# Kernel optimization log

Hardware: AMD Instinct MI355X
Metric: run time of the kernel (lower is better)

## Reference

```python
import jax, jax.numpy as jnp
import numpy as np

N, E, D, H, ED = 50000, 800000, 128, 4, 64
C = D // H  # per-head channels
EPS = 1e-5


def setup_inputs() -> dict:
    key = jax.random.key(0)
    ks = jax.random.split(key, 16)
    s = 0.05
    return {
        "x": jax.random.normal(ks[0], (N, D), jnp.float32),
        "edge_index": jax.random.randint(ks[1], (2, E), 0, N, jnp.int64 if jax.config.jax_enable_x64 else jnp.int32),
        "edge_attr": jax.random.normal(ks[2], (E, ED), jnp.float32),
        "Wq": jax.random.normal(ks[3], (D, H * C), jnp.float32) * s,
        "bq": jnp.zeros((H * C,), jnp.float32),
        "Wk": jax.random.normal(ks[4], (D, H * C), jnp.float32) * s,
        "bk": jnp.zeros((H * C,), jnp.float32),
        "Wv": jax.random.normal(ks[5], (D, H * C), jnp.float32) * s,
        "bv": jnp.zeros((H * C,), jnp.float32),
        "We": jax.random.normal(ks[6], (ED, H * C), jnp.float32) * s,  # lin_edge, bias=False
        "Wskip": jax.random.normal(ks[7], (D, H * C), jnp.float32) * s,
        "bskip": jnp.zeros((H * C,), jnp.float32),
        "Wbeta": jax.random.normal(ks[8], (3 * H * C, 1), jnp.float32) * s,  # lin_beta, bias=False
        "gamma": jnp.ones((D,), jnp.float32),
        "beta_ln": jnp.zeros((D,), jnp.float32),
    }


def _transformer_conv(x, src, dst, edge_attr, Wq, bq, Wk, bk, Wv, bv, We, Wskip, bskip, Wbeta):
    q = (x @ Wq + bq).reshape(N, H, C)
    k = (x @ Wk + bk).reshape(N, H, C)
    v = (x @ Wv + bv).reshape(N, H, C)
    e = (edge_attr @ We).reshape(E, H, C)
    k_j = k[src] + e                     # [E,H,C]
    v_j = v[src] + e                     # [E,H,C]
    alpha = jnp.einsum("ehc,ehc->eh", q[dst], k_j) / jnp.sqrt(jnp.float32(C))
    # per-destination softmax over incoming edges
    m = jax.ops.segment_max(alpha, dst, num_segments=N)          # [N,H]
    m = jnp.where(jnp.isfinite(m), m, 0.0)
    a = jnp.exp(alpha - m[dst])
    denom = jax.ops.segment_sum(a, dst, num_segments=N)          # [N,H]
    alpha = a / jnp.where(denom > 0, denom, 1.0)[dst]
    out = jax.ops.segment_sum(alpha[:, :, None] * v_j, dst, num_segments=N)  # [N,H,C]
    out = out.reshape(N, H * C)
    # beta-gated skip (beta=True, root_weight)
    x_r = x @ Wskip + bskip
    b = jax.nn.sigmoid(jnp.concatenate([out, x_r, out - x_r], axis=-1) @ Wbeta)  # [N,1]
    return b * x_r + (1.0 - b) * out


def reference(x, edge_index, edge_attr, Wq, bq, Wk, bk, Wv, bv, We, Wskip, bskip, Wbeta, gamma, beta_ln):
    src, dst = edge_index[0], edge_index[1]
    res = _transformer_conv(x, src, dst, edge_attr, Wq, bq, Wk, bk, Wv, bv, We, Wskip, bskip, Wbeta)
    out = jax.nn.gelu(res, approximate=False) + x
    mu = jnp.mean(out, axis=-1, keepdims=True)
    var = jnp.var(out, axis=-1, keepdims=True)
    return (out - mu) * jax.lax.rsqrt(var + EPS) * gamma + beta_ln
```

## Files before the change

kernel.cpp:

```cpp
#include <hip/hip_runtime.h>
#include <math.h>

#define NN 50000
#define EE 800000

typedef __bf16 bf16x8 __attribute__((ext_vector_type(8)));
typedef float f32x4 __attribute__((ext_vector_type(4)));
typedef float f32x2 __attribute__((ext_vector_type(2)));
typedef unsigned short ushort_t;
typedef unsigned int uint_t;

__device__ inline ushort_t f2bf(float f) {
  uint_t u = __float_as_uint(f);
  uint_t r = (u + 0x7fffu + ((u >> 16) & 1u)) >> 16;
  return (ushort_t)r;
}
__device__ inline float bflo(uint_t u) { return __uint_as_float(u << 16); }
__device__ inline float bfhi(uint_t u) { return __uint_as_float(u & 0xffff0000u); }

__device__ inline uint_t pk4_fp8(float a0, float a1, float a2, float a3) {
  a0 = fminf(fmaxf(a0, -448.f), 448.f);
  a1 = fminf(fmaxf(a1, -448.f), 448.f);
  a2 = fminf(fmaxf(a2, -448.f), 448.f);
  a3 = fminf(fmaxf(a3, -448.f), 448.f);
  uint_t lo = (uint_t)__builtin_amdgcn_cvt_pk_fp8_f32(a0, a1, 0, false) & 0xFFFFu;
  uint_t hi = (uint_t)__builtin_amdgcn_cvt_pk_fp8_f32(a2, a3, 0, false) & 0xFFFFu;
  return lo | (hi << 16);
}

__device__ inline void wave_sync() {
  asm volatile("s_waitcnt lgkmcnt(0)" ::: "memory");
  __builtin_amdgcn_wave_barrier();
}

__global__ __launch_bounds__(256) void k_prepA(const float* __restrict__ Wbeta,
                                               float* __restrict__ wcomb,
                                               int* __restrict__ counts) {
  int b = blockIdx.x;
  int o = threadIdx.x;
  if (b == 0) {
    if (o < 128) {
      wcomb[o]       = Wbeta[o]       + Wbeta[256 + o];
      wcomb[128 + o] = Wbeta[128 + o] - Wbeta[256 + o];
    }
  } else {
    int i = (b - 1) * 256 + o;
    if (i < NN) counts[i] = 0;
  }
}

__global__ __launch_bounds__(256) void k_prepB(
    const float* __restrict__ Wq, const float* __restrict__ Wk,
    const float* __restrict__ Wv, const float* __restrict__ Ws,
    const float* __restrict__ bq, const float* __restrict__ bk,
    const float* __restrict__ bv, const float* __restrict__ bs,
    ushort_t* __restrict__ Wbt, float* __restrict__ bcat,
    const float* __restrict__ We, ushort_t* __restrict__ WebT,
    const int* __restrict__ ei, int* __restrict__ counts,
    int* __restrict__ rank) {
  int b = blockIdx.x;
  if (b >= 288) {
    int i = (b - 288) * 256 + threadIdx.x;
    if (i < EE) rank[i] = atomicAdd(&counts[ei[EE + i]], 1);
    return;
  }
  if (b >= 256) {
    int i = (b - 256) * 256 + threadIdx.x;
    int c = i >> 6, k = i & 63;
    WebT[c * 64 + k] = f2bf(We[k * 128 + c]);
    return;
  }
  int i = b * 256 + threadIdx.x;
  int c = i >> 7, k = i & 127;
  float w;
  if (c < 128)      w = Wq[k * 128 + c];
  else if (c < 256) w = Wk[k * 128 + (c - 128)];
  else if (c < 384) w = Wv[k * 128 + (c - 256)];
  else              w = Ws[k * 128 + (c - 384)];
  Wbt[(size_t)c * 128 + k] = f2bf(w);
  if (i < 512) {
    float bb;
    if (i < 128)      bb = bq[i];
    else if (i < 256) bb = bk[i - 128];
    else if (i < 384) bb = bv[i - 256];
    else              bb = bs[i - 384];
    bcat[i] = bb;
  }
}

__global__ __launch_bounds__(256) void k_mmscan(const float* __restrict__ x,
                                                const ushort_t* __restrict__ Wbt,
                                                const float* __restrict__ bcat,
                                                ushort_t* __restrict__ qb,
                                                ushort_t* __restrict__ kb,
                                                ushort_t* __restrict__ vb,
                                                ushort_t* __restrict__ xrb,
                                                int* __restrict__ counts,
                                                int* __restrict__ offsets) {
  __shared__ ushort_t As[128 * 128];
  __shared__ ushort_t Bs[128 * 128];
  int t = threadIdx.x;

  if (blockIdx.x == 391) {
    if (blockIdx.y != 0) return;
    __shared__ int wsum[4];
    __shared__ int s_carry;
    int4* counts4 = (int4*)counts;
    int4* offsets4 = (int4*)offsets;
    int lane = t & 63, w = t >> 6;
    if (t == 0) s_carry = 0;
    __syncthreads();
    for (int base = 0; base < 12500; base += 256) {
      int idx = base + t;
      int4 v = (idx < 12500) ? counts4[idx] : make_int4(0, 0, 0, 0);
      int e1 = v.x, e2 = e1 + v.y, e3 = e2 + v.z, tot = e3 + v.w;
      int s = tot;
#pragma unroll
      for (int off = 1; off < 64; off <<= 1) {
        int u = __shfl_up(s, off);
        if (lane >= off) s += u;
      }
      if (lane == 63) wsum[w] = s;
      __syncthreads();
      if (t == 0) {
        int ex = s_carry;
#pragma unroll
        for (int i = 0; i < 4; ++i) { int tv = wsum[i]; wsum[i] = ex; ex += tv; }
        s_carry = ex;
      }
      __syncthreads();
      int be = wsum[w] + s - tot;
      if (idx < 12500) offsets4[idx] = make_int4(be, be + e1, be + e2, be + e3);
      __syncthreads();
    }
    if (t == 0) offsets[NN] = s_carry;
    return;
  }

  int rb = blockIdx.x * 128;
  int cb = blockIdx.y * 128;

  for (int q = t; q < 2048; q += 256) {
    int r = q >> 4, j = q & 15;
    int row = rb + r;
    float4 f0 = make_float4(0.f, 0.f, 0.f, 0.f), f1 = f0;
    if (row < NN) {
      const float4* xp = (const float4*)&x[(size_t)row * 128 + j * 8];
      f0 = xp[0]; f1 = xp[1];
    }
    uint_t u0 = (uint_t)f2bf(f0.x) | ((uint_t)f2bf(f0.y) << 16);
    uint_t u1 = (uint_t)f2bf(f0.z) | ((uint_t)f2bf(f0.w) << 16);
    uint_t u2 = (uint_t)f2bf(f1.x) | ((uint_t)f2bf(f1.y) << 16);
    uint_t u3 = (uint_t)f2bf(f1.z) | ((uint_t)f2bf(f1.w) << 16);
    int e = r * 128 + ((j * 8) ^ ((r & 7) << 3));
    *(uint4*)&As[e] = make_uint4(u0, u1, u2, u3);
  }
  for (int q = t; q < 2048; q += 256) {
    int c = q >> 4, j = q & 15;
    uint4 w = *(const uint4*)&Wbt[(size_t)(cb + c) * 128 + j * 8];
    int e = c * 128 + ((j * 8) ^ ((c & 7) << 3));
    *(uint4*)&Bs[e] = w;
  }
  __syncthreads();

  int lane = t & 63;
  int wv = t >> 6;
  int wr = wv >> 1, wc = wv & 1;
  int l15 = lane & 15, l4 = lane >> 4;

  f32x4 acc[4][4];
#pragma unroll
  for (int i = 0; i < 4; ++i)
#pragma unroll
    for (int j = 0; j < 4; ++j) acc[i][j] = (f32x4){0.f, 0.f, 0.f, 0.f};

#pragma unroll
  for (int ks = 0; ks < 4; ++ks) {
    int kbv = ks * 32 + l4 * 8;
    bf16x8 af[4], bfr[4];
#pragma unroll
    for (int i = 0; i < 4; ++i) {
      int r = wr * 64 + i * 16 + l15;
      af[i] = *(const bf16x8*)&As[r * 128 + (kbv ^ ((r & 7) << 3))];
    }
#pragma unroll
    for (int j = 0; j < 4; ++j) {
      int c = wc * 64 + j * 16 + l15;
      bfr[j] = *(const bf16x8*)&Bs[c * 128 + (kbv ^ ((c & 7) << 3))];
    }
#pragma unroll
    for (int i = 0; i < 4; ++i)
#pragma unroll
      for (int j = 0; j < 4; ++j)
        acc[i][j] = __builtin_amdgcn_mfma_f32_16x16x32_bf16(af[i], bfr[j], acc[i][j], 0, 0, 0);
  }

  ushort_t* outp = (cb == 0) ? qb : (cb == 128) ? kb : (cb == 256) ? vb : xrb;
#pragma unroll
  for (int j = 0; j < 4; ++j) {
    int colg = wc * 64 + j * 16 + l15;
    float bv = bcat[cb + colg];
#pragma unroll
    for (int i = 0; i < 4; ++i) {
#pragma unroll
      for (int reg = 0; reg < 4; ++reg) {
        int grow = rb + wr * 64 + i * 16 + l4 * 4 + reg;
        if (grow < NN)
          outp[(size_t)grow * 128 + colg] = f2bf(acc[i][j][reg] + bv);
      }
    }
  }
}

__global__ __launch_bounds__(256) void k_fillw(const int* __restrict__ ei,
                                               const int* __restrict__ offsets,
                                               const int* __restrict__ rank,
                                               const float* __restrict__ ea,
                                               const ushort_t* __restrict__ WebT,
                                               int* __restrict__ srcs,
                                               unsigned char* __restrict__ eaWperm) {
  __shared__ ushort_t Bs[128 * 64];
  __shared__ uint_t sOut[64 * 32];
  __shared__ int sP[128];
  int t = threadIdx.x, lane = t & 63, wv = t >> 6;
  int l15 = lane & 15, l4 = lane >> 4;
  int eb = blockIdx.x * 128;

  float4 ld[2][2][2];
#pragma unroll
  for (int T = 0; T < 2; ++T)
#pragma unroll
    for (int ks = 0; ks < 2; ++ks) {
      const float4* p4 = (const float4*)(ea + (size_t)(eb + T * 64 + wv * 16 + l15) * 64
                                         + ks * 32 + l4 * 8);
      ld[T][ks][0] = p4[0];
      ld[T][ks][1] = p4[1];
    }

  if (t < 128) {
    int e = eb + t;
    int d = ei[EE + e];
    int p = offsets[d] + rank[e];
    sP[t] = p;
    srcs[p] = ei[e];
  }
  for (int q = t; q < 1024; q += 256) {
    int c = q >> 3, j = q & 7;
    uint4 w = *(const uint4*)&WebT[(size_t)c * 64 + j * 8];
    *(uint4*)&Bs[c * 64 + ((j * 8) ^ ((c & 7) << 3))] = w;
  }
  __syncthreads();

#pragma unroll
  for (int T = 0; T < 2; ++T) {
    bf16x8 bfr[2];
#pragma unroll
    for (int ks = 0; ks < 2; ++ks) {
      float4 f0 = ld[T][ks][0], f1 = ld[T][ks][1];
      union { uint4 u; bf16x8 v; } ub;
      ub.u.x = (uint_t)f2bf(f0.x) | ((uint_t)f2bf(f0.y) << 16);
      ub.u.y = (uint_t)f2bf(f0.z) | ((uint_t)f2bf(f0.w) << 16);
      ub.u.z = (uint_t)f2bf(f1.x) | ((uint_t)f2bf(f1.y) << 16);
      ub.u.w = (uint_t)f2bf(f1.z) | ((uint_t)f2bf(f1.w) << 16);
      bfr[ks] = ub.v;
    }

    f32x4 acc[8];
#pragma unroll
    for (int i = 0; i < 8; ++i) acc[i] = (f32x4){0.f, 0.f, 0.f, 0.f};
#pragma unroll
    for (int ks = 0; ks < 2; ++ks) {
      int kbv = ks * 32 + l4 * 8;
#pragma unroll
      for (int i = 0; i < 8; ++i) {
        int c = i * 16 + l15;
        bf16x8 af = *(const bf16x8*)&Bs[c * 64 + (kbv ^ ((c & 7) << 3))];
        acc[i] = __builtin_amdgcn_mfma_f32_16x16x32_bf16(af, bfr[ks], acc[i], 0, 0, 0);
      }
    }

    wave_sync();
    uint_t* dst32 = &sOut[wv * 512];
#pragma unroll
    for (int i = 0; i < 8; ++i)
      dst32[l15 * 32 + ((i * 4 + l4) ^ ((l15 & 7) << 2))] =
          pk4_fp8(acc[i][0], acc[i][1], acc[i][2], acc[i][3]);
    wave_sync();

    int elr = lane >> 2, seg = lane & 3;
    int sw = (elr & 7) << 2;
    const uint_t* src32 = &sOut[wv * 512 + elr * 32];
    int w0 = (seg * 8) ^ sw;
    int w1 = (seg * 8 + 4) ^ sw;
    uint4 lo = *(const uint4*)&src32[w0];
    uint4 hi = *(const uint4*)&src32[w1];
    int p = sP[T * 64 + wv * 16 + elr];
    unsigned char* dst = eaWperm + (size_t)p * 128 + seg * 32;
    *(uint4*)dst = lo;
    *(uint4*)(dst + 16) = hi;
  }
}

__global__ __launch_bounds__(256) void k_attn(
    const ushort_t* __restrict__ qb, const ushort_t* __restrict__ xrb,
    const ushort_t* __restrict__ kb, const ushort_t* __restrict__ vb,
    const unsigned char* __restrict__ eaWperm,
    const int* __restrict__ offsets, const int* __restrict__ srcs,
    const float* __restrict__ x, const float* __restrict__ wcomb,
    const float* __restrict__ gamma, const float* __restrict__ beta_ln,
    float* __restrict__ out) {
  __shared__ float sQ[4][128];
  __shared__ unsigned char sEA[4][16][144];
  __shared__ float sA[4][64];
  __shared__ int   sS[4][16];

  int t = threadIdx.x, wv = t >> 6, l = t & 63;
  int n = blockIdx.x * 4 + wv;
  int h = l >> 4, m = l & 15;
  int c0 = 2 * l, c1 = c0 + 1;
  const float scale = 0.17677669529663687f;

  uint_t qw = *(const uint_t*)&qb[(size_t)n * 128 + c0];
  *(float2*)&sQ[wv][c0] = make_float2(bflo(qw) * scale, bfhi(qw) * scale);
  if (l < 16) sS[wv][l] = 0;

  int js = offsets[n], je = offsets[n + 1];
  float acc0 = 0.f, acc1 = 0.f, lsum = 0.f;

  uint4 e0 = {0,0,0,0}, e1 = {0,0,0,0};
  uint4 k0 = {0,0,0,0}, k1 = {0,0,0,0}, k2 = {0,0,0,0}, k3 = {0,0,0,0};
  int scur = 0;
  if (m < je - js) {
    scur = srcs[js + m];
    const uint4* erow = (const uint4*)(eaWperm + (size_t)(js + m) * 128 + 32 * h);
    e0 = erow[0]; e1 = erow[1];
    const uint4* krow = (const uint4*)(kb + (size_t)scur * 128 + 32 * h);
    k0 = krow[0]; k1 = krow[1]; k2 = krow[2]; k3 = krow[3];
  }

  for (int base = js; base < je; base += 16) {
    int nj = je - base; if (nj > 16) nj = 16;
    wave_sync();

    *(uint4*)&sEA[wv][m][32 * h]      = e0;
    *(uint4*)&sEA[wv][m][32 * h + 16] = e1;
    if (h == 0) sS[wv][m] = scur;

    uint4 ne0 = {0,0,0,0}, ne1 = {0,0,0,0};
    uint4 nk0 = {0,0,0,0}, nk1 = {0,0,0,0}, nk2 = {0,0,0,0}, nk3 = {0,0,0,0};
    int snx = 0;
    int nb = base + 16;
    if (nb < je && m < je - nb) {
      snx = srcs[nb + m];
      const uint4* erow = (const uint4*)(eaWperm + (size_t)(nb + m) * 128 + 32 * h);
      ne0 = erow[0]; ne1 = erow[1];
      const uint4* krow = (const uint4*)(kb + (size_t)snx * 128 + 32 * h);
      nk0 = krow[0]; nk1 = krow[1]; nk2 = krow[2]; nk3 = krow[3];
    }
    wave_sync();

    int4 s0 = *(const int4*)&sS[wv][0];
    int4 s1 = *(const int4*)&sS[wv][4];
    int4 s2 = *(const int4*)&sS[wv][8];
    int4 s3 = *(const int4*)&sS[wv][12];
    uint_t vva[8], vvb[8];
    {
      int sidx[8] = {s0.x, s0.y, s0.z, s0.w, s1.x, s1.y, s1.z, s1.w};
#pragma unroll
      for (int e = 0; e < 8; ++e)
        vva[e] = *(const uint_t*)(vb + (size_t)sidx[e] * 128 + c0);
    }
    {
      int sidx[8] = {s2.x, s2.y, s2.z, s2.w, s3.x, s3.y, s3.z, s3.w};
#pragma unroll
      for (int e = 0; e < 8; ++e)
        vvb[e] = *(const uint_t*)(vb + (size_t)sidx[e] * 128 + c0);
    }

    float z = 0.f;
    {
      const float* qp = &sQ[wv][32 * h];
      uint_t eu[8] = {e0.x, e0.y, e0.z, e0.w, e1.x, e1.y, e1.z, e1.w};
      uint_t ku[16] = {k0.x, k0.y, k0.z, k0.w, k1.x, k1.y, k1.z, k1.w,
                       k2.x, k2.y, k2.z, k2.w, k3.x, k3.y, k3.z, k3.w};
#pragma unroll
      for (int u = 0; u < 8; ++u) {
        f32x2 elo = __builtin_amdgcn_cvt_pk_f32_fp8(eu[u] & 0xFFFFu, false);
        f32x2 ehi = __builtin_amdgcn_cvt_pk_f32_fp8(eu[u] >> 16, false);
        float4 q4 = *(const float4*)&qp[4 * u];
        z += q4.x * (bflo(ku[2 * u]) + elo.x)
           + q4.y * (bfhi(ku[2 * u]) + elo.y)
           + q4.z * (bflo(ku[2 * u + 1]) + ehi.x)
           + q4.w * (bfhi(ku[2 * u + 1]) + ehi.y);
      }
    }
    float a = (m < nj) ? __expf(z) : 0.0f;
    lsum += a;
    sA[wv][l] = a;
    wave_sync();

    {
      f32x4 a0 = *(const f32x4*)&sA[wv][16 * h];
      f32x4 a1 = *(const f32x4*)&sA[wv][16 * h + 4];
#pragma unroll
      for (int e = 0; e < 8; ++e) {
        float ae = (e < 4) ? a0[e] : a1[e - 4];
        uint_t ew = (uint_t)*(const ushort_t*)&sEA[wv][e][2 * l];
        f32x2 ef = __builtin_amdgcn_cvt_pk_f32_fp8(ew, false);
        acc0 += ae * (bflo(vva[e]) + ef.x);
        acc1 += ae * (bfhi(vva[e]) + ef.y);
      }
    }
    if (nj > 8) {
      f32x4 a2 = *(const f32x4*)&sA[wv][16 * h + 8];
      f32x4 a3 = *(const f32x4*)&sA[wv][16 * h + 12];
#pragma unroll
      for (int e = 0; e < 8; ++e) {
        float ae = (e < 4) ? a2[e] : a3[e - 4];
        uint_t ew = (uint_t)*(const ushort_t*)&sEA[wv][8 + e][2 * l];
        f32x2 ef = __builtin_amdgcn_cvt_pk_f32_fp8(ew, false);
        acc0 += ae * (bflo(vvb[e]) + ef.x);
        acc1 += ae * (bfhi(vvb[e]) + ef.y);
      }
    }

    e0 = ne0; e1 = ne1; k0 = nk0; k1 = nk1; k2 = nk2; k3 = nk3; scur = snx;
  }

  lsum += __shfl_xor(lsum, 1); lsum += __shfl_xor(lsum, 2);
  lsum += __shfl_xor(lsum, 4); lsum += __shfl_xor(lsum, 8);

  float inv = (lsum > 0.f) ? (1.0f / lsum) : 1.0f;
  float o0 = acc0 * inv;
  float o1 = acc1 * inv;

  uint_t xw = *(const uint_t*)&xrb[(size_t)n * 128 + c0];
  float2 xrv = make_float2(bflo(xw), bfhi(xw));
  float bp = o0 * wcomb[c0] + o1 * wcomb[c1] + xrv.x * wcomb[128 + c0] + xrv.y * wcomb[128 + c1];
#pragma unroll
  for (int off = 32; off > 0; off >>= 1) bp += __shfl_xor(bp, off);
  float bgate = 1.0f / (1.0f + __expf(-bp));
  float r0 = bgate * xrv.x + (1.0f - bgate) * o0;
  float r1 = bgate * xrv.y + (1.0f - bgate) * o1;

  float2 xv = *(const float2*)&x[(size_t)n * 128 + c0];
  float ge0 = 0.5f * r0 * (1.0f + erff(r0 * 0.70710678118654752f)) + xv.x;
  float ge1 = 0.5f * r1 * (1.0f + erff(r1 * 0.70710678118654752f)) + xv.y;

  float s1 = ge0 + ge1;
  float s2 = ge0 * ge0 + ge1 * ge1;
#pragma unroll
  for (int off = 32; off > 0; off >>= 1) {
    s1 += __shfl_xor(s1, off);
    s2 += __shfl_xor(s2, off);
  }
  float mean = s1 * (1.0f / 128.0f);
  float var = s2 * (1.0f / 128.0f) - mean * mean;
  float rstd = rsqrtf(var + 1e-5f);
  float2 ov;
  ov.x = (ge0 - mean) * rstd * gamma[c0] + beta_ln[c0];
  ov.y = (ge1 - mean) * rstd * gamma[c1] + beta_ln[c1];
  *(float2*)&out[(size_t)n * 128 + c0] = ov;
}

extern "C" void kernel_launch(void* const* d_in, const int* in_sizes, int n_in,
                              void* d_out, int out_size, void* d_ws, size_t ws_size,
                              hipStream_t stream) {
  const float* x   = (const float*)d_in[0];
  const int*   ei  = (const int*)d_in[1];
  const float* ea  = (const float*)d_in[2];
  const float* Wq  = (const float*)d_in[3];
  const float* bq  = (const float*)d_in[4];
  const float* Wk  = (const float*)d_in[5];
  const float* bk  = (const float*)d_in[6];
  const float* Wv  = (const float*)d_in[7];
  const float* bv  = (const float*)d_in[8];
  const float* We  = (const float*)d_in[9];
  const float* Wsk = (const float*)d_in[10];
  const float* bsk = (const float*)d_in[11];
  const float* Wb  = (const float*)d_in[12];
  const float* gamma = (const float*)d_in[13];
  const float* beta  = (const float*)d_in[14];
  float* out = (float*)d_out;

  char* cur = (char*)d_ws;
  auto alloc = [&](size_t bytes) {
    void* p = (void*)cur;
    cur += (bytes + 255) & ~(size_t)255;
    return p;
  };
  ushort_t*      qbuf    = (ushort_t*)alloc((size_t)NN * 128 * 2);
  ushort_t*      kbuf    = (ushort_t*)alloc((size_t)NN * 128 * 2);
  ushort_t*      vbuf    = (ushort_t*)alloc((size_t)NN * 128 * 2);
  ushort_t*      xrbuf   = (ushort_t*)alloc((size_t)NN * 128 * 2);
  unsigned char* eaWperm = (unsigned char*)alloc((size_t)EE * 128);
  int*           srcs    = (int*)alloc((size_t)EE * 4);
  int*           rank    = (int*)alloc((size_t)EE * 4);
  float*         wcomb   = (float*)alloc(256 * 4);
  float*         bcat    = (float*)alloc(512 * 4);
  ushort_t*      Wbt     = (ushort_t*)alloc((size_t)512 * 128 * 2);
  ushort_t*      WebT    = (ushort_t*)alloc((size_t)128 * 64 * 2);
  int*           counts  = (int*)alloc((size_t)NN * 4);
  int*           offsets = (int*)alloc((size_t)(NN + 4) * 4);

  k_prepA<<<197, 256, 0, stream>>>(Wb, wcomb, counts);
  k_prepB<<<288 + 3125, 256, 0, stream>>>(Wq, Wk, Wv, Wsk, bq, bk, bv, bsk,
                                          Wbt, bcat, We, WebT, ei, counts, rank);
  k_mmscan<<<dim3(392, 4), 256, 0, stream>>>(x, Wbt, bcat, qbuf, kbuf, vbuf,
                                             xrbuf, counts, offsets);
  k_fillw<<<6250, 256, 0, stream>>>(ei, offsets, rank, ea, WebT, srcs, eaWperm);
  k_attn<<<12500, 256, 0, stream>>>(qbuf, xrbuf, kbuf, vbuf, eaWperm, offsets,
                                    srcs, x, wcomb, gamma, beta, out);
}
```

Measured before the change: 276.9 us.

## Split scan into standalone kernel and fuse node GEMM with edge-fill kernel

The prefix scan over destination counts moves out of the GEMM kernel into its own single-block kernel with 1024 threads. The node QKV/skip GEMM is retiled from 128x128 to 64x64 tiles and merged into one launch with the edge-projection/permutation fill, sharing shared memory through a union. The aim is to drop the serial scan block from the GEMM critical path, let GEMM blocks run alongside fill blocks, and raise occupancy through smaller tiles. The cost is an extra single-block launch that serializes before the fused kernel, plus less operand reuse per GEMM tile.

```diff
diff --git a/kernel.cpp b/kernel.cpp
--- a/kernel.cpp
+++ b/kernel.cpp
@@ -88,59 +88,141 @@
   }
 }
 
-__global__ __launch_bounds__(256) void k_mmscan(const float* __restrict__ x,
-                                                const ushort_t* __restrict__ Wbt,
-                                                const float* __restrict__ bcat,
-                                                ushort_t* __restrict__ qb,
-                                                ushort_t* __restrict__ kb,
-                                                ushort_t* __restrict__ vb,
-                                                ushort_t* __restrict__ xrb,
-                                                int* __restrict__ counts,
-                                                int* __restrict__ offsets) {
-  __shared__ ushort_t As[128 * 128];
-  __shared__ ushort_t Bs[128 * 128];
-  int t = threadIdx.x;
-
-  if (blockIdx.x == 391) {
-    if (blockIdx.y != 0) return;
-    __shared__ int wsum[4];
-    __shared__ int s_carry;
-    int4* counts4 = (int4*)counts;
-    int4* offsets4 = (int4*)offsets;
-    int lane = t & 63, w = t >> 6;
-    if (t == 0) s_carry = 0;
+__global__ __launch_bounds__(1024) void k_scan(int* __restrict__ counts, int* __restrict__ offsets) {
+  __shared__ int wsum[16];
+  __shared__ int s_carry;
+  int4* counts4 = (int4*)counts;
+  int4* offsets4 = (int4*)offsets;
+  int t = threadIdx.x, lane = t & 63, w = t >> 6;
+  if (t == 0) s_carry = 0;
+  __syncthreads();
+  for (int base = 0; base < 12500; base += 1024) {
+    int idx = base + t;
+    int4 v = (idx < 12500) ? counts4[idx] : make_int4(0, 0, 0, 0);
+    int e1 = v.x, e2 = e1 + v.y, e3 = e2 + v.z, tot = e3 + v.w;
+    int s = tot;
+#pragma unroll
+    for (int off = 1; off < 64; off <<= 1) {
+      int u = __shfl_up(s, off);
+      if (lane >= off) s += u;
+    }
+    if (lane == 63) wsum[w] = s;
     __syncthreads();
-    for (int base = 0; base < 12500; base += 256) {
-      int idx = base + t;
-      int4 v = (idx < 12500) ? counts4[idx] : make_int4(0, 0, 0, 0);
-      int e1 = v.x, e2 = e1 + v.y, e3 = e2 + v.z, tot = e3 + v.w;
-      int s = tot;
-#pragma unroll
-      for (int off = 1; off < 64; off <<= 1) {
-        int u = __shfl_up(s, off);
-        if (lane >= off) s += u;
-      }
-      if (lane == 63) wsum[w] = s;
-      __syncthreads();
-      if (t == 0) {
-        int ex = s_carry;
-#pragma unroll
-        for (int i = 0; i < 4; ++i) { int tv = wsum[i]; wsum[i] = ex; ex += tv; }
-        s_carry = ex;
-      }
-      __syncthreads();
-      int be = wsum[w] + s - tot;
-      if (idx < 12500) offsets4[idx] = make_int4(be, be + e1, be + e2, be + e3);
-      __syncthreads();
-    }
-    if (t == 0) offsets[NN] = s_carry;
+    if (t == 0) {
+      int ex = s_carry;
+#pragma unroll
+      for (int i = 0; i < 16; ++i) { int tv = wsum[i]; wsum[i] = ex; ex += tv; }
+      s_carry = ex;
+    }
+    __syncthreads();
+    int excl = wsum[w] + s - tot;
+    if (idx < 12500) offsets4[idx] = make_int4(excl, excl + e1, excl + e2, excl + e3);
+    __syncthreads();
+  }
+  if (t == 0) offsets[NN] = s_carry;
+}
+
+#define NBFILL 6250
+__global__ __launch_bounds__(256) void k_mmfill(
+    const int* __restrict__ ei, const int* __restrict__ offsets,
+    const int* __restrict__ rank, const float* __restrict__ ea,
+    const ushort_t* __restrict__ WebT, int* __restrict__ srcs,
+    unsigned char* __restrict__ eaWperm,
+    const float* __restrict__ x, const ushort_t* __restrict__ Wbt,
+    const float* __restrict__ bcat, ushort_t* __restrict__ qb,
+    ushort_t* __restrict__ kb, ushort_t* __restrict__ vb,
+    ushort_t* __restrict__ xrb) {
+  __shared__ union {
+    struct { ushort_t As[64 * 128]; ushort_t Bs[64 * 128]; } mm;
+    struct { ushort_t Bs[128 * 64]; uint_t sOut[64 * 32]; int sP[128]; } fw;
+  } U;
+  int t = threadIdx.x, lane = t & 63, wv = t >> 6;
+  int l15 = lane & 15, l4 = lane >> 4;
+
+  if (blockIdx.x < NBFILL) {
+    int eb = blockIdx.x * 128;
+
+    float4 ld[2][2][2];
+#pragma unroll
+    for (int T = 0; T < 2; ++T)
+#pragma unroll
+      for (int ks = 0; ks < 2; ++ks) {
+        const float4* p4 = (const float4*)(ea + (size_t)(eb + T * 64 + wv * 16 + l15) * 64
+                                           + ks * 32 + l4 * 8);
+        ld[T][ks][0] = p4[0];
+        ld[T][ks][1] = p4[1];
+      }
+
+    if (t < 128) {
+      int e = eb + t;
+      int d = ei[EE + e];
+      int p = offsets[d] + rank[e];
+      U.fw.sP[t] = p;
+      srcs[p] = ei[e];
+    }
+    for (int q = t; q < 1024; q += 256) {
+      int c = q >> 3, j = q & 7;
+      uint4 w = *(const uint4*)&WebT[(size_t)c * 64 + j * 8];
+      *(uint4*)&U.fw.Bs[c * 64 + ((j * 8) ^ ((c & 7) << 3))] = w;
+    }
+    __syncthreads();
+
+#pragma unroll
+    for (int T = 0; T < 2; ++T) {
+      bf16x8 bfr[2];
+#pragma unroll
+      for (int ks = 0; ks < 2; ++ks) {
+        float4 f0 = ld[T][ks][0], f1 = ld[T][ks][1];
+        union { uint4 u; bf16x8 v; } ub;
+        ub.u.x = (uint_t)f2bf(f0.x) | ((uint_t)f2bf(f0.y) << 16);
+        ub.u.y = (uint_t)f2bf(f0.z) | ((uint_t)f2bf(f0.w) << 16);
+        ub.u.z = (uint_t)f2bf(f1.x) | ((uint_t)f2bf(f1.y) << 16);
+        ub.u.w = (uint_t)f2bf(f1.z) | ((uint_t)f2bf(f1.w) << 16);
+        bfr[ks] = ub.v;
+      }
+
+      f32x4 acc[8];
+#pragma unroll
+      for (int i = 0; i < 8; ++i) acc[i] = (f32x4){0.f, 0.f, 0.f, 0.f};
+#pragma unroll
+      for (int ks = 0; ks < 2; ++ks) {
+        int kbv = ks * 32 + l4 * 8;
+#pragma unroll
+        for (int i = 0; i < 8; ++i) {
+          int c = i * 16 + l15;
+          bf16x8 af = *(const bf16x8*)&U.fw.Bs[c * 64 + (kbv ^ ((c & 7) << 3))];
+          acc[i] = __builtin_amdgcn_mfma_f32_16x16x32_bf16(af, bfr[ks], acc[i], 0, 0, 0);
+        }
+      }
+
+      wave_sync();
+      uint_t* dst32 = &U.fw.sOut[wv * 512];
+#pragma unroll
+      for (int i = 0; i < 8; ++i)
+        dst32[l15 * 32 + ((i * 4 + l4) ^ ((l15 & 7) << 2))] =
+            pk4_fp8(acc[i][0], acc[i][1], acc[i][2], acc[i][3]);
+      wave_sync();
+
+      int elr = lane >> 2, seg = lane & 3;
+      int sw = (elr & 7) << 2;
+      const uint_t* src32 = &U.fw.sOut[wv * 512 + elr * 32];
+      int w0 = (seg * 8) ^ sw;
+      int w1 = (seg * 8 + 4) ^ sw;
+      uint4 lo = *(const uint4*)&src32[w0];
+      uint4 hi = *(const uint4*)&src32[w1];
+      int p = U.fw.sP[T * 64 + wv * 16 + elr];
+      unsigned char* dst = eaWperm + (size_t)p * 128 + seg * 32;
+      *(uint4*)dst = lo;
+      *(uint4*)(dst + 16) = hi;
+    }
     return;
   }
 
-  int rb = blockIdx.x * 128;
-  int cb = blockIdx.y * 128;
-
-  for (int q = t; q < 2048; q += 256) {
+  int mb = blockIdx.x - NBFILL;
+  int rb = (mb >> 3) * 64;
+  int cb = (mb & 7) * 64;
+
+  for (int q = t; q < 1024; q += 256) {
     int r = q >> 4, j = q & 15;
     int row = rb + r;
     float4 f0 = make_float4(0.f, 0.f, 0.f, 0.f), f1 = f0;
@@ -153,151 +235,60 @@
     uint_t u2 = (uint_t)f2bf(f1.x) | ((uint_t)f2bf(f1.y) << 16);
     uint_t u3 = (uint_t)f2bf(f1.z) | ((uint_t)f2bf(f1.w) << 16);
     int e = r * 128 + ((j * 8) ^ ((r & 7) << 3));
-    *(uint4*)&As[e] = make_uint4(u0, u1, u2, u3);
-  }
-  for (int q = t; q < 2048; q += 256) {
+    *(uint4*)&U.mm.As[e] = make_uint4(u0, u1, u2, u3);
+  }
+  for (int q = t; q < 1024; q += 256) {
     int c = q >> 4, j = q & 15;
     uint4 w = *(const uint4*)&Wbt[(size_t)(cb + c) * 128 + j * 8];
     int e = c * 128 + ((j * 8) ^ ((c & 7) << 3));
-    *(uint4*)&Bs[e] = w;
+    *(uint4*)&U.mm.Bs[e] = w;
   }
   __syncthreads();
 
-  int lane = t & 63;
-  int wv = t >> 6;
   int wr = wv >> 1, wc = wv & 1;
-  int l15 = lane & 15, l4 = lane >> 4;
-
-  f32x4 acc[4][4];
-#pragma unroll
-  for (int i = 0; i < 4; ++i)
-#pragma unroll
-    for (int j = 0; j < 4; ++j) acc[i][j] = (f32x4){0.f, 0.f, 0.f, 0.f};
+
+  f32x4 acc[2][2];
+#pragma unroll
+  for (int i = 0; i < 2; ++i)
+#pragma unroll
+    for (int j = 0; j < 2; ++j) acc[i][j] = (f32x4){0.f, 0.f, 0.f, 0.f};
 
 #pragma unroll
   for (int ks = 0; ks < 4; ++ks) {
     int kbv = ks * 32 + l4 * 8;
-    bf16x8 af[4], bfr[4];
-#pragma unroll
-    for (int i = 0; i < 4; ++i) {
-      int r = wr * 64 + i * 16 + l15;
-      af[i] = *(const bf16x8*)&As[r * 128 + (kbv ^ ((r & 7) << 3))];
-    }
-#pragma unroll
-    for (int j = 0; j < 4; ++j) {
-      int c = wc * 64 + j * 16 + l15;
-      bfr[j] = *(const bf16x8*)&Bs[c * 128 + (kbv ^ ((c & 7) << 3))];
-    }
-#pragma unroll
-    for (int i = 0; i < 4; ++i)
-#pragma unroll
-      for (int j = 0; j < 4; ++j)
+    bf16x8 af[2], bfr[2];
+#pragma unroll
+    for (int i = 0; i < 2; ++i) {
+      int r = wr * 32 + i * 16 + l15;
+      af[i] = *(const bf16x8*)&U.mm.As[r * 128 + (kbv ^ ((r & 7) << 3))];
+    }
+#pragma unroll
+    for (int j = 0; j < 2; ++j) {
+      int c = wc * 32 + j * 16 + l15;
+      bfr[j] = *(const bf16x8*)&U.mm.Bs[c * 128 + (kbv ^ ((c & 7) << 3))];
+    }
+#pragma unroll
+    for (int i = 0; i < 2; ++i)
+#pragma unroll
+      for (int j = 0; j < 2; ++j)
         acc[i][j] = __builtin_amdgcn_mfma_f32_16x16x32_bf16(af[i], bfr[j], acc[i][j], 0, 0, 0);
   }
 
-  ushort_t* outp = (cb == 0) ? qb : (cb == 128) ? kb : (cb == 256) ? vb : xrb;
-#pragma unroll
-  for (int j = 0; j < 4; ++j) {
-    int colg = wc * 64 + j * 16 + l15;
-    float bv = bcat[cb + colg];
-#pragma unroll
-    for (int i = 0; i < 4; ++i) {
+#pragma unroll
+  for (int j = 0; j < 2; ++j) {
+    int colg = cb + wc * 32 + j * 16 + l15;
+    float bv = bcat[colg];
+    ushort_t* outp = (colg < 128) ? qb : (colg < 256) ? kb : (colg < 384) ? vb : xrb;
+    int cc = colg & 127;
+#pragma unroll
+    for (int i = 0; i < 2; ++i) {
 #pragma unroll
       for (int reg = 0; reg < 4; ++reg) {
-        int grow = rb + wr * 64 + i * 16 + l4 * 4 + reg;
+        int grow = rb + wr * 32 + i * 16 + l4 * 4 + reg;
         if (grow < NN)
-          outp[(size_t)grow * 128 + colg] = f2bf(acc[i][j][reg] + bv);
-      }
-    }
-  }
-}
-
-__global__ __launch_bounds__(256) void k_fillw(const int* __restrict__ ei,
-                                               const int* __restrict__ offsets,
-                                               const int* __restrict__ rank,
-                                               const float* __restrict__ ea,
-                                               const ushort_t* __restrict__ WebT,
-                                               int* __restrict__ srcs,
-                                               unsigned char* __restrict__ eaWperm) {
-  __shared__ ushort_t Bs[128 * 64];
-  __shared__ uint_t sOut[64 * 32];
-  __shared__ int sP[128];
-  int t = threadIdx.x, lane = t & 63, wv = t >> 6;
-  int l15 = lane & 15, l4 = lane >> 4;
-  int eb = blockIdx.x * 128;
-
-  float4 ld[2][2][2];
-#pragma unroll
-  for (int T = 0; T < 2; ++T)
-#pragma unroll
-    for (int ks = 0; ks < 2; ++ks) {
-      const float4* p4 = (const float4*)(ea + (size_t)(eb + T * 64 + wv * 16 + l15) * 64
-                                         + ks * 32 + l4 * 8);
-      ld[T][ks][0] = p4[0];
-      ld[T][ks][1] = p4[1];
-    }
-
-  if (t < 128) {
-    int e = eb + t;
-    int d = ei[EE + e];
-    int p = offsets[d] + rank[e];
-    sP[t] = p;
-    srcs[p] = ei[e];
-  }
-  for (int q = t; q < 1024; q += 256) {
-    int c = q >> 3, j = q & 7;
-    uint4 w = *(const uint4*)&WebT[(size_t)c * 64 + j * 8];
-    *(uint4*)&Bs[c * 64 + ((j * 8) ^ ((c & 7) << 3))] = w;
-  }
-  __syncthreads();
-
-#pragma unroll
-  for (int T = 0; T < 2; ++T) {
-    bf16x8 bfr[2];
-#pragma unroll
-    for (int ks = 0; ks < 2; ++ks) {
-      float4 f0 = ld[T][ks][0], f1 = ld[T][ks][1];
-      union { uint4 u; bf16x8 v; } ub;
-      ub.u.x = (uint_t)f2bf(f0.x) | ((uint_t)f2bf(f0.y) << 16);
-      ub.u.y = (uint_t)f2bf(f0.z) | ((uint_t)f2bf(f0.w) << 16);
-      ub.u.z = (uint_t)f2bf(f1.x) | ((uint_t)f2bf(f1.y) << 16);
-      ub.u.w = (uint_t)f2bf(f1.z) | ((uint_t)f2bf(f1.w) << 16);
-      bfr[ks] = ub.v;
-    }
-
-    f32x4 acc[8];
-#pragma unroll
-    for (int i = 0; i < 8; ++i) acc[i] = (f32x4){0.f, 0.f, 0.f, 0.f};
-#pragma unroll
-    for (int ks = 0; ks < 2; ++ks) {
-      int kbv = ks * 32 + l4 * 8;
-#pragma unroll
-      for (int i = 0; i < 8; ++i) {
-        int c = i * 16 + l15;
-        bf16x8 af = *(const bf16x8*)&Bs[c * 64 + (kbv ^ ((c & 7) << 3))];
-        acc[i] = __builtin_amdgcn_mfma_f32_16x16x32_bf16(af, bfr[ks], acc[i], 0, 0, 0);
-      }
-    }
-
-    wave_sync();
-    uint_t* dst32 = &sOut[wv * 512];
-#pragma unroll
-    for (int i = 0; i < 8; ++i)
-      dst32[l15 * 32 + ((i * 4 + l4) ^ ((l15 & 7) << 2))] =
-          pk4_fp8(acc[i][0], acc[i][1], acc[i][2], acc[i][3]);
-    wave_sync();
-
-    int elr = lane >> 2, seg = lane & 3;
-    int sw = (elr & 7) << 2;
-    const uint_t* src32 = &sOut[wv * 512 + elr * 32];
-    int w0 = (seg * 8) ^ sw;
-    int w1 = (seg * 8 + 4) ^ sw;
-    uint4 lo = *(const uint4*)&src32[w0];
-    uint4 hi = *(const uint4*)&src32[w1];
-    int p = sP[T * 64 + wv * 16 + elr];
-    unsigned char* dst = eaWperm + (size_t)p * 128 + seg * 32;
-    *(uint4*)dst = lo;
-    *(uint4*)(dst + 16) = hi;
+          outp[(size_t)grow * 128 + cc] = f2bf(acc[i][j][reg] + bv);
+      }
+    }
   }
 }
 
@@ -506,9 +497,10 @@
   k_prepA<<<197, 256, 0, stream>>>(Wb, wcomb, counts);
   k_prepB<<<288 + 3125, 256, 0, stream>>>(Wq, Wk, Wv, Wsk, bq, bk, bv, bsk,
                                           Wbt, bcat, We, WebT, ei, counts, rank);
-  k_mmscan<<<dim3(392, 4), 256, 0, stream>>>(x, Wbt, bcat, qbuf, kbuf, vbuf,
-                                             xrbuf, counts, offsets);
-  k_fillw<<<6250, 256, 0, stream>>>(ei, offsets, rank, ea, WebT, srcs, eaWperm);
+  k_scan<<<1, 1024, 0, stream>>>(counts, offsets);
+  k_mmfill<<<NBFILL + 6256, 256, 0, stream>>>(ei, offsets, rank, ea, WebT, srcs,
+                                              eaWperm, x, Wbt, bcat, qbuf, kbuf,
+                                              vbuf, xrbuf);
   k_attn<<<12500, 256, 0, stream>>>(qbuf, xrbuf, kbuf, vbuf, eaWperm, offsets,
                                     srcs, x, wcomb, gamma, beta, out);
 }
```

Measured after the change: 284.4 us. 2.7% more time.
